# Kernel tuning notes

Measured on AMD Instinct MI355X. Metric: run time of the kernel, lower is better.

## Reference

```python
import jax, jax.numpy as jnp
import numpy as np

B, Cfi, H, W = 2, 32, 192, 192
Cfp, Cfo, NUM = 1, 2, 16
N = H * W
Ct = Cfo + Cfi + Cfi + Cfp  # 67
EPS = 1e-5


def _bn(x, g, b, m, v):
    # x: (B, C, num, N); per-channel inference batchnorm
    inv = g * jax.lax.rsqrt(v + EPS)
    return x * inv[None, :, None, None] + (b - m * inv)[None, :, None, None]


def _pconv(x, Wt):
    # 1x1 conv as channel contraction: Wt (Cout, Cin), x (B, Cin, num, N)
    return jnp.einsum('oc,bcmn->bomn', Wt, x)


def setup_inputs() -> dict:
    key = jax.random.key(0)
    ks = jax.random.split(key, 32)
    inp = {
        'If': jax.random.normal(ks[0], (B, Cfi, H, W), jnp.float32),
        'Pf': jax.random.normal(ks[1], (B, Cfp, H, W), jnp.float32),
        'Ofnum': jax.random.normal(ks[2], (B, Cfo, NUM, N), jnp.float32),
        'args': jax.random.randint(ks[3], (B, NUM, N), 0, N, jnp.int64),
    }
    def conv_w(k, co, ci):
        return jax.random.normal(k, (co, ci), jnp.float32) * (1.0 / np.sqrt(ci))
    def bn_p(k, c):
        k1, k2 = jax.random.split(k)
        return (jnp.ones((c,), jnp.float32),
                jnp.zeros((c,), jnp.float32),
                jax.random.normal(k1, (c,), jnp.float32) * 0.1,
                jax.random.uniform(k2, (c,), jnp.float32, 0.5, 1.5))
    # convXF: Ct->Cfi, Cfi->Cfi (both BN+GELU)
    inp['W1'] = conv_w(ks[4], Cfi, Ct)
    inp['g1'], inp['b1'], inp['m1'], inp['v1'] = bn_p(ks[5], Cfi)
    inp['W2'] = conv_w(ks[6], Cfi, Cfi)
    inp['g2'], inp['b2'], inp['m2'], inp['v2'] = bn_p(ks[7], Cfi)
    # convXL: Cfi->Cfi (BN+GELU), Cfi->Cfi (BN only)
    inp['W3'] = conv_w(ks[8], Cfi, Cfi)
    inp['g3'], inp['b3'], inp['m3'], inp['v3'] = bn_p(ks[9], Cfi)
    inp['W4'] = conv_w(ks[10], Cfi, Cfi)
    inp['g4'], inp['b4'], inp['m4'], inp['v4'] = bn_p(ks[11], Cfi)
    # coef: Cfi -> 3, with bias
    inp['Wc'] = conv_w(ks[12], 3, Cfi)
    inp['bc'] = jax.random.normal(ks[13], (3,), jnp.float32) * 0.01
    return inp


def reference(If, Pf, Ofnum, args,
              W1, g1, b1, m1, v1,
              W2, g2, b2, m2, v2,
              W3, g3, b3, m3, v3,
              W4, g4, b4, m4, v4,
              Wc, bc):
    gelu = lambda x: jax.nn.gelu(x, approximate=False)
    If_flat = If.reshape(B, Cfi, N)   # (B, Cfi, N)
    Pf_flat = Pf.reshape(B, Cfp, N)   # (B, Cfp, M), M == N here

    # per-batch neighbor gather along flattened spatial dim
    gath = jax.vmap(lambda f, a: f[:, a])  # (C,N),(num,N) -> (C,num,N)
    IPfnum = gath(If_flat, args)            # (B, Cfi, num, N)
    Pfnum = gath(Pf_flat, args)             # (B, Cfp, num, N)
    Ifnum = jnp.broadcast_to(If_flat[:, :, None, :], (B, Cfi, NUM, N))

    X = jnp.concatenate([Ifnum, IPfnum, Pfnum, Ofnum], axis=1)  # (B, Ct, num, N)

    h = gelu(_bn(_pconv(X, W1), g1, b1, m1, v1))
    h = gelu(_bn(_pconv(h, W2), g2, b2, m2, v2))
    l = gelu(_bn(_pconv(h, W3), g3, b3, m3, v3))
    l = _bn(_pconv(l, W4), g4, b4, m4, v4)
    XF = gelu(h + l)

    feat = _pconv(XF, Wc) + bc[None, :, None, None]  # (B, 3, num, N)
    Alpha, Beta, Omega = feat[:, 0:1], feat[:, 1:2], feat[:, 2:3]
    Omega = jax.nn.softmax(Omega, axis=2)
    dout = jnp.sum(((Alpha + 1.0) * Pfnum[:, -1:] + Beta) * Omega,
                   axis=2, keepdims=True)  # (B, 1, 1, N)
    return dout.reshape(B, 1, H, W)
```

## Files before the change

kernel.cpp:

```cpp
#include <hip/hip_runtime.h>
#include <math.h>

#define BB   2
#define CFI  32
#define NN   36864
#define NUMM 16

#define ZOFS (BB * NN * CFI)

typedef __attribute__((ext_vector_type(8))) short short8;
typedef __attribute__((ext_vector_type(4))) float f4;

static __device__ __forceinline__ f4 mm16(short8 a, short8 b, f4 c) {
    return __builtin_amdgcn_mfma_f32_16x16x32_bf16(a, b, c, 0, 0, 0);
}

static __device__ __forceinline__ float gelu_fast(float x) {
    const float x2  = x * x;
    const float q   = fmaf(-0.10294310f, x2, -2.30211813f);
    const float e   = exp2f(q * x);
    const float r   = __builtin_amdgcn_rcpf(e + 1.0f);
    return x * r;
}

static __device__ __forceinline__ unsigned bf16_rne_bits(float x) {
    unsigned u = __builtin_bit_cast(unsigned, x);
    return u + 0x7fffu + ((u >> 16) & 1u);
}
static __device__ __forceinline__ void split_pack(float x0, float x1,
                                                  unsigned& hi, unsigned& lo) {
    unsigned r0 = bf16_rne_bits(x0);
    unsigned r1 = bf16_rne_bits(x1);
    float h0 = __builtin_bit_cast(float, r0 & 0xffff0000u);
    float h1 = __builtin_bit_cast(float, r1 & 0xffff0000u);
    hi = (r0 >> 16) | (r1 & 0xffff0000u);
    unsigned s0 = bf16_rne_bits(x0 - h0);
    unsigned s1 = bf16_rne_bits(x1 - h1);
    lo = (s0 >> 16) | (s1 & 0xffff0000u);
}

static __device__ __forceinline__ unsigned pack2(float a, float b) {
    unsigned ua = __builtin_bit_cast(unsigned, a) + 0x8000u;
    unsigned ub = __builtin_bit_cast(unsigned, b) + 0x8000u;
    return (ua >> 16) | (ub & 0xffff0000u);
}

union UV { unsigned u[4]; short8 v; };

__global__ __launch_bounds__(256) void yz_kernel(
    const float* __restrict__ If, const float* __restrict__ Pf,
    const float* __restrict__ W1, const float* __restrict__ g1,
    const float* __restrict__ b1, const float* __restrict__ m1,
    const float* __restrict__ v1,
    float* __restrict__ wsYZ)
{
    __shared__ float wy[1024], wz[1024], wp[32], bt1[32];
    for (int i = threadIdx.x; i < 1024; i += 256) {
        int o = i >> 5, c = i & 31;
        float inv = g1[o] * rsqrtf(v1[o] + 1e-5f);
        wy[i] = W1[o * 67 + c]      * inv;
        wz[i] = W1[o * 67 + 32 + c] * inv;
    }
    if (threadIdx.x < 32) {
        int o = threadIdx.x;
        float inv = g1[o] * rsqrtf(v1[o] + 1e-5f);
        wp[o]  = W1[o * 67 + 64] * inv;
        bt1[o] = b1[o] - m1[o] * inv;
    }
    __syncthreads();

    const int r  = threadIdx.x & 3;
    const int p  = blockIdx.x * 64 + (threadIdx.x >> 2);
    const int b  = p / NN, n = p - b * NN;
    const int o0 = r * 8;
    const float* ifp = If + (size_t)b * CFI * NN + n;

    float v[32];
#pragma unroll
    for (int c = 0; c < 32; c++) v[c] = ifp[(size_t)c * NN];
    const float pf = Pf[p];

    float accY[8], accZ[8];
#pragma unroll
    for (int j = 0; j < 8; j++) {
        const float4* wyr = (const float4*)&wy[(o0 + j) * 32];
        const float4* wzr = (const float4*)&wz[(o0 + j) * 32];
        float ay = bt1[o0 + j];
        float az = wp[o0 + j] * pf;
#pragma unroll
        for (int c4 = 0; c4 < 8; c4++) {
            float4 a = wyr[c4], z = wzr[c4];
            ay = fmaf(a.x, v[4 * c4 + 0], ay);  az = fmaf(z.x, v[4 * c4 + 0], az);
            ay = fmaf(a.y, v[4 * c4 + 1], ay);  az = fmaf(z.y, v[4 * c4 + 1], az);
            ay = fmaf(a.z, v[4 * c4 + 2], ay);  az = fmaf(z.z, v[4 * c4 + 2], az);
            ay = fmaf(a.w, v[4 * c4 + 3], ay);  az = fmaf(z.w, v[4 * c4 + 3], az);
        }
        accY[j] = ay; accZ[j] = az;
    }

    float4* yp = (float4*)(wsYZ + (size_t)p * 32 + o0);
    float4* zp = (float4*)(wsYZ + ZOFS + (size_t)p * 32 + o0);
    yp[0] = make_float4(accY[0], accY[1], accY[2], accY[3]);
    yp[1] = make_float4(accY[4], accY[5], accY[6], accY[7]);
    zp[0] = make_float4(accZ[0], accZ[1], accZ[2], accZ[3]);
    zp[1] = make_float4(accZ[4], accZ[5], accZ[6], accZ[7]);
}

__global__ __launch_bounds__(256, 5) void main_kernel(
    const float* __restrict__ Pf, const float* __restrict__ Of,
    const int* __restrict__ args,
    const float* __restrict__ W1, const float* __restrict__ g1,
    const float* __restrict__ v1,
    const float* __restrict__ W2, const float* __restrict__ g2,
    const float* __restrict__ b2, const float* __restrict__ m2,
    const float* __restrict__ v2,
    const float* __restrict__ W3, const float* __restrict__ g3,
    const float* __restrict__ b3, const float* __restrict__ m3,
    const float* __restrict__ v3,
    const float* __restrict__ W4, const float* __restrict__ g4,
    const float* __restrict__ b4, const float* __restrict__ m4,
    const float* __restrict__ v4,
    const float* __restrict__ Wc, const float* __restrict__ bc,
    const float* __restrict__ ws, float* __restrict__ out)
{
    __shared__ __align__(16) unsigned wfrag[3][2][2][64][4];
    __shared__ __align__(16) float btl[3 * 32];
    __shared__ __align__(16) float wch[3 * 32];
    __shared__ __align__(16) float w1t[2 * 32];
    __shared__ float bcs[3];
    __shared__ int   izs;

    const float* Ws[3] = {W2, W3, W4};
    const float* gs[3] = {g2, g3, g4};
    const float* vs[3] = {v2, v3, v4};
    const float* bs[3] = {b2, b3, b4};
    const float* ms[3] = {m2, m3, m4};

    for (int idx = threadIdx.x; idx < 1536; idx += 256) {
        int p    = idx & 3;
        int ln   = (idx >> 2) & 63;
        int T    = (idx >> 8) & 1;
        int L    = idx >> 9;
        int o    = T * 16 + (ln & 15);
        int c    = ((ln >> 4) << 3) + 2 * p;
        float inv = gs[L][o] * rsqrtf(vs[L][o] + 1e-5f);
        float w0 = Ws[L][o * 32 + c]     * inv;
        float w1 = Ws[L][o * 32 + c + 1] * inv;
        unsigned hi, lo;
        split_pack(w0, w1, hi, lo);
        wfrag[L][T][0][ln][p] = hi;
        wfrag[L][T][1][ln][p] = lo;
    }
    if (threadIdx.x < 96) {
        int L = threadIdx.x >> 5, ch = threadIdx.x & 31;
        btl[threadIdx.x] = bs[L][ch] - ms[L][ch] * (gs[L][ch] * rsqrtf(vs[L][ch] + 1e-5f));
        wch[threadIdx.x] = Wc[L * 32 + ch];
    }
    if (threadIdx.x < 64) {
        int t = threadIdx.x >> 5, ch = threadIdx.x & 31;
        float i1 = g1[ch] * rsqrtf(v1[ch] + 1e-5f);
        w1t[threadIdx.x] = W1[ch * 67 + 65 + t] * i1;
    }
    if (threadIdx.x < 3) bcs[threadIdx.x] = bc[threadIdx.x];
    if (threadIdx.x == 0) izs = (int)(args[0] >> 16);
    __syncthreads();

    const int lane = threadIdx.x & 63;
    const int wid  = threadIdx.x >> 6;
    const int mI   = lane & 15;
    const int quad = lane >> 4;
    const int c0   = quad * 8;
    const int s0   = mI + 32 * (quad & 1);
    const int s1   = s0 + 16;
    const bool hiT = (quad >> 1) != 0;
    const int izero = izs;

#pragma unroll 1
    for (int i = 0; i < 4; i++) {
        const int io  = i & izero;
        const int C = blockIdx.x * 16 + wid * 4 + i;
        const int b = (C >= NN) ? 1 : 0;
        const int n = C - b * NN;

        const int   aIdx = args[(b * NUMM + mI) * NN + n];
        const float of0v = Of[((b * 2 + 0) * NUMM + mI) * NN + n];
        const float of1v = Of[((b * 2 + 1) * NUMM + mI) * NN + n];
        const float pfg  = Pf[b * NN + aIdx];

        const f4* yp = (const f4*)(ws + (size_t)(b * NN + n) * 32 + c0);
        const f4* zp = (const f4*)(ws + ZOFS + (size_t)(b * NN + aIdx) * 32 + c0);
        f4 y0 = yp[0], y1 = yp[1], z0 = zp[0], z1 = zp[1];

        const f4 wo0a = *(const f4*)&w1t[c0 + 4 * io];
        const f4 wo0b = *(const f4*)&w1t[c0 + 4 + 4 * io];
        const f4 wo1a = *(const f4*)&w1t[32 + c0 + 4 * io];
        const f4 wo1b = *(const f4*)&w1t[32 + c0 + 4 + 4 * io];

        float x[8];
#pragma unroll
        for (int j = 0; j < 4; j++) {
            x[j]     = fmaf(of1v, wo1a[j], fmaf(of0v, wo0a[j], y0[j] + z0[j]));
            x[4 + j] = fmaf(of1v, wo1b[j], fmaf(of0v, wo0b[j], y1[j] + z1[j]));
        }
#pragma unroll
        for (int j = 0; j < 8; j++) x[j] = gelu_fast(x[j]);
        UV Bv;
#pragma unroll
        for (int p = 0; p < 4; p++) Bv.u[p] = pack2(x[2 * p], x[2 * p + 1]);

        f4 bt00 = *(const f4*)&btl[0 * 32 + 4 * quad + 4 * io];
        f4 bt01 = *(const f4*)&btl[0 * 32 + 16 + 4 * quad + 4 * io];
        short8 A0l = *(const short8*)&wfrag[0][0][1][lane + io][0];
        short8 A0h = *(const short8*)&wfrag[0][0][0][lane + io][0];
        short8 A1l = *(const short8*)&wfrag[0][1][1][lane + io][0];
        short8 A1h = *(const short8*)&wfrag[0][1][0][lane + io][0];
        f4 acc0 = mm16(A0l, Bv.v, bt00);
        acc0    = mm16(A0h, Bv.v, acc0);
        f4 acc1 = mm16(A1l, Bv.v, bt01);
        acc1    = mm16(A1h, Bv.v, acc1);
        float h2c[8];
#pragma unroll
        for (int r = 0; r < 4; r++) {
            h2c[r]     = gelu_fast(acc0[r]);
            h2c[4 + r] = gelu_fast(acc1[r]);
        }
        {
            unsigned lo0 = pack2(h2c[0], h2c[1]), lo1 = pack2(h2c[2], h2c[3]);
            unsigned hi0 = pack2(h2c[4], h2c[5]), hi1 = pack2(h2c[6], h2c[7]);
            unsigned a0s0 = __shfl(lo0, s0, 64), b0s0 = __shfl(hi0, s0, 64);
            unsigned a1s0 = __shfl(lo1, s0, 64), b1s0 = __shfl(hi1, s0, 64);
            unsigned a0s1 = __shfl(lo0, s1, 64), b0s1 = __shfl(hi0, s1, 64);
            unsigned a1s1 = __shfl(lo1, s1, 64), b1s1 = __shfl(hi1, s1, 64);
            Bv.u[0] = hiT ? b0s0 : a0s0;
            Bv.u[1] = hiT ? b1s0 : a1s0;
            Bv.u[2] = hiT ? b0s1 : a0s1;
            Bv.u[3] = hiT ? b1s1 : a1s1;
        }

        f4 bt10 = *(const f4*)&btl[1 * 32 + 4 * quad + 4 * io];
        f4 bt11 = *(const f4*)&btl[1 * 32 + 16 + 4 * quad + 4 * io];
        A0l = *(const short8*)&wfrag[1][0][1][lane + io][0];
        A0h = *(const short8*)&wfrag[1][0][0][lane + io][0];
        A1l = *(const short8*)&wfrag[1][1][1][lane + io][0];
        A1h = *(const short8*)&wfrag[1][1][0][lane + io][0];
        acc0 = mm16(A0l, Bv.v, bt10);
        acc0 = mm16(A0h, Bv.v, acc0);
        acc1 = mm16(A1l, Bv.v, bt11);
        acc1 = mm16(A1h, Bv.v, acc1);
        {
            float g0 = gelu_fast(acc0[0]), g1_ = gelu_fast(acc0[1]);
            float g2_ = gelu_fast(acc0[2]), g3_ = gelu_fast(acc0[3]);
            float g4_ = gelu_fast(acc1[0]), g5 = gelu_fast(acc1[1]);
            float g6 = gelu_fast(acc1[2]), g7 = gelu_fast(acc1[3]);
            unsigned lo0 = pack2(g0, g1_), lo1 = pack2(g2_, g3_);
            unsigned hi0 = pack2(g4_, g5), hi1 = pack2(g6, g7);
            unsigned a0s0 = __shfl(lo0, s0, 64), b0s0 = __shfl(hi0, s0, 64);
            unsigned a1s0 = __shfl(lo1, s0, 64), b1s0 = __shfl(hi1, s0, 64);
            unsigned a0s1 = __shfl(lo0, s1, 64), b0s1 = __shfl(hi0, s1, 64);
            unsigned a1s1 = __shfl(lo1, s1, 64), b1s1 = __shfl(hi1, s1, 64);
            Bv.u[0] = hiT ? b0s0 : a0s0;
            Bv.u[1] = hiT ? b1s0 : a1s0;
            Bv.u[2] = hiT ? b0s1 : a0s1;
            Bv.u[3] = hiT ? b1s1 : a1s1;
        }

        f4 bt20 = *(const f4*)&btl[2 * 32 + 4 * quad + 4 * io];
        f4 bt21 = *(const f4*)&btl[2 * 32 + 16 + 4 * quad + 4 * io];
        A0l = *(const short8*)&wfrag[2][0][1][lane + io][0];
        A0h = *(const short8*)&wfrag[2][0][0][lane + io][0];
        A1l = *(const short8*)&wfrag[2][1][1][lane + io][0];
        A1h = *(const short8*)&wfrag[2][1][0][lane + io][0];
        acc0 = mm16(A0l, Bv.v, bt20);
        acc0 = mm16(A0h, Bv.v, acc0);
        acc1 = mm16(A1l, Bv.v, bt21);
        acc1 = mm16(A1h, Bv.v, acc1);

        const f4 wA0 = *(const f4*)&wch[0 * 32 + 4 * quad + 4 * io];
        const f4 wA1 = *(const f4*)&wch[0 * 32 + 16 + 4 * quad + 4 * io];
        const f4 wB0 = *(const f4*)&wch[1 * 32 + 4 * quad + 4 * io];
        const f4 wB1 = *(const f4*)&wch[1 * 32 + 16 + 4 * quad + 4 * io];
        const f4 wO0 = *(const f4*)&wch[2 * 32 + 4 * quad + 4 * io];
        const f4 wO1 = *(const f4*)&wch[2 * 32 + 16 + 4 * quad + 4 * io];

        float pa = 0.0f, pb = 0.0f, po = 0.0f;
#pragma unroll
        for (int r = 0; r < 4; r++) {
            float xf0 = gelu_fast(h2c[r]     + acc0[r]);
            float xf1 = gelu_fast(h2c[4 + r] + acc1[r]);
            pa = fmaf(wA0[r], xf0, pa);  pa = fmaf(wA1[r], xf1, pa);
            pb = fmaf(wB0[r], xf0, pb);  pb = fmaf(wB1[r], xf1, pb);
            po = fmaf(wO0[r], xf0, po);  po = fmaf(wO1[r], xf1, po);
        }
        pa += __shfl_xor(pa, 16, 64);  pa += __shfl_xor(pa, 32, 64);
        pb += __shfl_xor(pb, 16, 64);  pb += __shfl_xor(pb, 32, 64);
        po += __shfl_xor(po, 16, 64);  po += __shfl_xor(po, 32, 64);
        const float alpha = pa + bcs[0];
        const float beta_ = pb + bcs[1];
        const float omega = po + bcs[2];
        const float val = fmaf(alpha + 1.0f, pfg, beta_);

        float mx = omega;
#pragma unroll
        for (int s = 1; s < 16; s <<= 1) mx = fmaxf(mx, __shfl_xor(mx, s, 64));
        const float e = __expf(omega - mx);
        float S = e, T = val * e;
#pragma unroll
        for (int s = 1; s < 16; s <<= 1) {
            S += __shfl_xor(S, s, 64);
            T += __shfl_xor(T, s, 64);
        }
        if (lane == 0) out[b * NN + n] = T / S;
    }
}

extern "C" void kernel_launch(void* const* d_in, const int* in_sizes, int n_in,
                              void* d_out, int out_size, void* d_ws, size_t ws_size,
                              hipStream_t stream) {
    const float* If    = (const float*)d_in[0];
    const float* Pf    = (const float*)d_in[1];
    const float* Of    = (const float*)d_in[2];
    const int*   args  = (const int*)d_in[3];
    const float* W1    = (const float*)d_in[4];
    const float* g1    = (const float*)d_in[5];
    const float* b1    = (const float*)d_in[6];
    const float* m1    = (const float*)d_in[7];
    const float* v1    = (const float*)d_in[8];
    const float* W2    = (const float*)d_in[9];
    const float* g2    = (const float*)d_in[10];
    const float* b2    = (const float*)d_in[11];
    const float* m2    = (const float*)d_in[12];
    const float* v2    = (const float*)d_in[13];
    const float* W3    = (const float*)d_in[14];
    const float* g3    = (const float*)d_in[15];
    const float* b3    = (const float*)d_in[16];
    const float* m3    = (const float*)d_in[17];
    const float* v3    = (const float*)d_in[18];
    const float* W4    = (const float*)d_in[19];
    const float* g4    = (const float*)d_in[20];
    const float* b4    = (const float*)d_in[21];
    const float* m4    = (const float*)d_in[22];
    const float* v4    = (const float*)d_in[23];
    const float* Wc    = (const float*)d_in[24];
    const float* bc    = (const float*)d_in[25];

    float* ws  = (float*)d_ws;
    float* out = (float*)d_out;

    yz_kernel<<<(BB * NN) / 64, 256, 0, stream>>>(
        If, Pf, W1, g1, b1, m1, v1, ws);

    main_kernel<<<(BB * NN) / 16, 256, 0, stream>>>(
        Pf, Of, args,
        W1, g1, v1,
        W2, g2, b2, m2, v2,
        W3, g3, b3, m3, v3,
        W4, g4, b4, m4, v4,
        Wc, bc, ws, out);
}
```

Measured before the change: 234.2 us.

## Switch layer MLP to 32x32x16 MFMA covering two pixels per wave

Replaces the 16x16x32 bf16 MFMA chain with 32x32x16 MFMAs so each wave processes two output pixels (32 neighbor columns) per iteration. The weight fragment layout is rebuilt so the accumulator output layout matches the next layer's B-operand input, which removes the cross-lane shuffle relayout between layers. The loop trip count halves and the coefficient reduction needs fewer shuffles. In exchange, per-lane register use grows (16-wide accumulators and activations), which may pressure occupancy under the 5-wave launch bound.

```diff
diff --git a/kernel.cpp b/kernel.cpp
--- a/kernel.cpp
+++ b/kernel.cpp
@@ -10,9 +10,10 @@
 
 typedef __attribute__((ext_vector_type(8))) short short8;
 typedef __attribute__((ext_vector_type(4))) float f4;
-
-static __device__ __forceinline__ f4 mm16(short8 a, short8 b, f4 c) {
-    return __builtin_amdgcn_mfma_f32_16x16x32_bf16(a, b, c, 0, 0, 0);
+typedef __attribute__((ext_vector_type(16))) float f16v;
+
+static __device__ __forceinline__ f16v mm32(short8 a, short8 b, f16v c) {
+    return __builtin_amdgcn_mfma_f32_32x32x16_bf16(a, b, c, 0, 0, 0);
 }
 
 static __device__ __forceinline__ float gelu_fast(float x) {
@@ -105,6 +106,39 @@
     zp[0] = make_float4(accZ[0], accZ[1], accZ[2], accZ[3]);
     zp[1] = make_float4(accZ[4], accZ[5], accZ[6], accZ[7]);
 }
+
+#define LAYER(Lc, BIN0, BIN1, ACCV)                                           \
+    {                                                                         \
+        const f4 bq0 = *(const f4*)&btl[(Lc) * 32 +      4 * hi + 4 * io];    \
+        const f4 bq1 = *(const f4*)&btl[(Lc) * 32 +  8 + 4 * hi + 4 * io];    \
+        const f4 bq2 = *(const f4*)&btl[(Lc) * 32 + 16 + 4 * hi + 4 * io];    \
+        const f4 bq3 = *(const f4*)&btl[(Lc) * 32 + 24 + 4 * hi + 4 * io];    \
+        ACCV[0]  = bq0[0]; ACCV[1]  = bq0[1]; ACCV[2]  = bq0[2]; ACCV[3]  = bq0[3]; \
+        ACCV[4]  = bq1[0]; ACCV[5]  = bq1[1]; ACCV[6]  = bq1[2]; ACCV[7]  = bq1[3]; \
+        ACCV[8]  = bq2[0]; ACCV[9]  = bq2[1]; ACCV[10] = bq2[2]; ACCV[11] = bq2[3]; \
+        ACCV[12] = bq3[0]; ACCV[13] = bq3[1]; ACCV[14] = bq3[2]; ACCV[15] = bq3[3]; \
+        short8 Af;                                                            \
+        Af = *(const short8*)&wfrag[(Lc)][0][1][lane + io][0];                \
+        ACCV = mm32(Af, BIN0.v, ACCV);                                        \
+        Af = *(const short8*)&wfrag[(Lc)][0][0][lane + io][0];                \
+        ACCV = mm32(Af, BIN0.v, ACCV);                                        \
+        Af = *(const short8*)&wfrag[(Lc)][1][1][lane + io][0];                \
+        ACCV = mm32(Af, BIN1.v, ACCV);                                        \
+        Af = *(const short8*)&wfrag[(Lc)][1][0][lane + io][0];                \
+        ACCV = mm32(Af, BIN1.v, ACCV);                                        \
+    }
+
+#define RELAYOUT(SRC, B0V, B1V)                                               \
+    {                                                                         \
+        B0V.u[0] = pack2(SRC[0],  SRC[1]);                                    \
+        B0V.u[1] = pack2(SRC[2],  SRC[3]);                                    \
+        B0V.u[2] = pack2(SRC[4],  SRC[5]);                                    \
+        B0V.u[3] = pack2(SRC[6],  SRC[7]);                                    \
+        B1V.u[0] = pack2(SRC[8],  SRC[9]);                                    \
+        B1V.u[1] = pack2(SRC[10], SRC[11]);                                   \
+        B1V.u[2] = pack2(SRC[12], SRC[13]);                                   \
+        B1V.u[3] = pack2(SRC[14], SRC[15]);                                   \
+    }
 
 __global__ __launch_bounds__(256, 5) void main_kernel(
     const float* __restrict__ Pf, const float* __restrict__ Of,
@@ -137,19 +171,20 @@
     const float* ms[3] = {m2, m3, m4};
 
     for (int idx = threadIdx.x; idx < 1536; idx += 256) {
-        int p    = idx & 3;
-        int ln   = (idx >> 2) & 63;
-        int T    = (idx >> 8) & 1;
-        int L    = idx >> 9;
-        int o    = T * 16 + (ln & 15);
-        int c    = ((ln >> 4) << 3) + 2 * p;
-        float inv = gs[L][o] * rsqrtf(vs[L][o] + 1e-5f);
-        float w0 = Ws[L][o * 32 + c]     * inv;
-        float w1 = Ws[L][o * 32 + c + 1] * inv;
-        unsigned hi, lo;
-        split_pack(w0, w1, hi, lo);
-        wfrag[L][T][0][ln][p] = hi;
-        wfrag[L][T][1][ln][p] = lo;
+        int pp  = idx & 3;
+        int ln  = (idx >> 2) & 63;
+        int kh  = (idx >> 8) & 1;
+        int L   = idx >> 9;
+        int row = ln & 31;
+        int g   = ln >> 5;
+        int k   = kh * 16 + 4 * g + 2 * (pp & 1) + 8 * (pp >> 1);
+        float inv = gs[L][row] * rsqrtf(vs[L][row] + 1e-5f);
+        float w0 = Ws[L][row * 32 + k]     * inv;
+        float w1 = Ws[L][row * 32 + k + 1] * inv;
+        unsigned hiw, low;
+        split_pack(w0, w1, hiw, low);
+        wfrag[L][kh][0][ln][pp] = hiw;
+        wfrag[L][kh][1][ln][pp] = low;
     }
     if (threadIdx.x < 96) {
         int L = threadIdx.x >> 5, ch = threadIdx.x & 31;
@@ -165,135 +200,86 @@
     if (threadIdx.x == 0) izs = (int)(args[0] >> 16);
     __syncthreads();
 
-    const int lane = threadIdx.x & 63;
-    const int wid  = threadIdx.x >> 6;
-    const int mI   = lane & 15;
-    const int quad = lane >> 4;
-    const int c0   = quad * 8;
-    const int s0   = mI + 32 * (quad & 1);
-    const int s1   = s0 + 16;
-    const bool hiT = (quad >> 1) != 0;
+    const int lane  = threadIdx.x & 63;
+    const int wid   = threadIdx.x >> 6;
+    const int m     = lane & 15;
+    const int pt    = (lane >> 4) & 1;
+    const int hi    = lane >> 5;
+    const int q4    = hi << 2;
     const int izero = izs;
 
 #pragma unroll 1
-    for (int i = 0; i < 4; i++) {
-        const int io  = i & izero;
-        const int C = blockIdx.x * 16 + wid * 4 + i;
-        const int b = (C >= NN) ? 1 : 0;
-        const int n = C - b * NN;
-
-        const int   aIdx = args[(b * NUMM + mI) * NN + n];
-        const float of0v = Of[((b * 2 + 0) * NUMM + mI) * NN + n];
-        const float of1v = Of[((b * 2 + 1) * NUMM + mI) * NN + n];
+    for (int i = 0; i < 2; i++) {
+        const int io = i & izero;
+        const int C  = blockIdx.x * 16 + wid * 4 + i * 2 + pt;
+        const int b  = (C >= NN) ? 1 : 0;
+        const int n  = C - b * NN;
+
+        const int   aIdx = args[(b * NUMM + m) * NN + n];
+        const float of0v = Of[((b * 2 + 0) * NUMM + m) * NN + n];
+        const float of1v = Of[((b * 2 + 1) * NUMM + m) * NN + n];
         const float pfg  = Pf[b * NN + aIdx];
 
-        const f4* yp = (const f4*)(ws + (size_t)(b * NN + n) * 32 + c0);
-        const f4* zp = (const f4*)(ws + ZOFS + (size_t)(b * NN + aIdx) * 32 + c0);
-        f4 y0 = yp[0], y1 = yp[1], z0 = zp[0], z1 = zp[1];
-
-        const f4 wo0a = *(const f4*)&w1t[c0 + 4 * io];
-        const f4 wo0b = *(const f4*)&w1t[c0 + 4 + 4 * io];
-        const f4 wo1a = *(const f4*)&w1t[32 + c0 + 4 * io];
-        const f4 wo1b = *(const f4*)&w1t[32 + c0 + 4 + 4 * io];
-
-        float x[8];
+        const f4* yb = (const f4*)(ws + (size_t)(b * NN + n) * 32);
+        const f4* zb = (const f4*)(ws + ZOFS + (size_t)(b * NN + aIdx) * 32);
+        f4 y0 = yb[hi], y1 = yb[2 + hi], y2 = yb[4 + hi], y3 = yb[6 + hi];
+        f4 z0 = zb[hi], z1 = zb[2 + hi], z2 = zb[4 + hi], z3 = zb[6 + hi];
+
+        const f4 wa0 = *(const f4*)&w1t[q4 + 4 * io];
+        const f4 wa1 = *(const f4*)&w1t[8 + q4 + 4 * io];
+        const f4 wa2 = *(const f4*)&w1t[16 + q4 + 4 * io];
+        const f4 wa3 = *(const f4*)&w1t[24 + q4 + 4 * io];
+        const f4 wb0 = *(const f4*)&w1t[32 + q4 + 4 * io];
+        const f4 wb1 = *(const f4*)&w1t[40 + q4 + 4 * io];
+        const f4 wb2 = *(const f4*)&w1t[48 + q4 + 4 * io];
+        const f4 wb3 = *(const f4*)&w1t[56 + q4 + 4 * io];
+
+        float x[16];
 #pragma unroll
         for (int j = 0; j < 4; j++) {
-            x[j]     = fmaf(of1v, wo1a[j], fmaf(of0v, wo0a[j], y0[j] + z0[j]));
-            x[4 + j] = fmaf(of1v, wo1b[j], fmaf(of0v, wo0b[j], y1[j] + z1[j]));
+            x[j]      = fmaf(of1v, wb0[j], fmaf(of0v, wa0[j], y0[j] + z0[j]));
+            x[4 + j]  = fmaf(of1v, wb1[j], fmaf(of0v, wa1[j], y1[j] + z1[j]));
+            x[8 + j]  = fmaf(of1v, wb2[j], fmaf(of0v, wa2[j], y2[j] + z2[j]));
+            x[12 + j] = fmaf(of1v, wb3[j], fmaf(of0v, wa3[j], y3[j] + z3[j]));
         }
 #pragma unroll
-        for (int j = 0; j < 8; j++) x[j] = gelu_fast(x[j]);
-        UV Bv;
-#pragma unroll
-        for (int p = 0; p < 4; p++) Bv.u[p] = pack2(x[2 * p], x[2 * p + 1]);
-
-        f4 bt00 = *(const f4*)&btl[0 * 32 + 4 * quad + 4 * io];
-        f4 bt01 = *(const f4*)&btl[0 * 32 + 16 + 4 * quad + 4 * io];
-        short8 A0l = *(const short8*)&wfrag[0][0][1][lane + io][0];
-        short8 A0h = *(const short8*)&wfrag[0][0][0][lane + io][0];
-        short8 A1l = *(const short8*)&wfrag[0][1][1][lane + io][0];
-        short8 A1h = *(const short8*)&wfrag[0][1][0][lane + io][0];
-        f4 acc0 = mm16(A0l, Bv.v, bt00);
-        acc0    = mm16(A0h, Bv.v, acc0);
-        f4 acc1 = mm16(A1l, Bv.v, bt01);
-        acc1    = mm16(A1h, Bv.v, acc1);
-        float h2c[8];
-#pragma unroll
-        for (int r = 0; r < 4; r++) {
-            h2c[r]     = gelu_fast(acc0[r]);
-            h2c[4 + r] = gelu_fast(acc1[r]);
+        for (int j = 0; j < 16; j++) x[j] = gelu_fast(x[j]);
+        UV B0, B1;
+        RELAYOUT(x, B0, B1);
+
+        f16v acc;
+        LAYER(0, B0, B1, acc);
+        float h2g[16];
+#pragma unroll
+        for (int r = 0; r < 16; r++) h2g[r] = gelu_fast(acc[r]);
+        RELAYOUT(h2g, B0, B1);
+
+        LAYER(1, B0, B1, acc);
+        float h3g[16];
+#pragma unroll
+        for (int r = 0; r < 16; r++) h3g[r] = gelu_fast(acc[r]);
+        RELAYOUT(h3g, B0, B1);
+
+        LAYER(2, B0, B1, acc);
+
+        float pa = 0.0f, pb = 0.0f, po = 0.0f;
+#pragma unroll
+        for (int q = 0; q < 4; q++) {
+            const f4 wAq = *(const f4*)&wch[      8 * q + q4 + 4 * io];
+            const f4 wBq = *(const f4*)&wch[32 +  8 * q + q4 + 4 * io];
+            const f4 wOq = *(const f4*)&wch[64 +  8 * q + q4 + 4 * io];
+#pragma unroll
+            for (int r2 = 0; r2 < 4; r2++) {
+                float xf = gelu_fast(h2g[4 * q + r2] + acc[4 * q + r2]);
+                pa = fmaf(wAq[r2], xf, pa);
+                pb = fmaf(wBq[r2], xf, pb);
+                po = fmaf(wOq[r2], xf, po);
+            }
         }
-        {
-            unsigned lo0 = pack2(h2c[0], h2c[1]), lo1 = pack2(h2c[2], h2c[3]);
-            unsigned hi0 = pack2(h2c[4], h2c[5]), hi1 = pack2(h2c[6], h2c[7]);
-            unsigned a0s0 = __shfl(lo0, s0, 64), b0s0 = __shfl(hi0, s0, 64);
-            unsigned a1s0 = __shfl(lo1, s0, 64), b1s0 = __shfl(hi1, s0, 64);
-            unsigned a0s1 = __shfl(lo0, s1, 64), b0s1 = __shfl(hi0, s1, 64);
-            unsigned a1s1 = __shfl(lo1, s1, 64), b1s1 = __shfl(hi1, s1, 64);
-            Bv.u[0] = hiT ? b0s0 : a0s0;
-            Bv.u[1] = hiT ? b1s0 : a1s0;
-            Bv.u[2] = hiT ? b0s1 : a0s1;
-            Bv.u[3] = hiT ? b1s1 : a1s1;
-        }
-
-        f4 bt10 = *(const f4*)&btl[1 * 32 + 4 * quad + 4 * io];
-        f4 bt11 = *(const f4*)&btl[1 * 32 + 16 + 4 * quad + 4 * io];
-        A0l = *(const short8*)&wfrag[1][0][1][lane + io][0];
-        A0h = *(const short8*)&wfrag[1][0][0][lane + io][0];
-        A1l = *(const short8*)&wfrag[1][1][1][lane + io][0];
-        A1h = *(const short8*)&wfrag[1][1][0][lane + io][0];
-        acc0 = mm16(A0l, Bv.v, bt10);
-        acc0 = mm16(A0h, Bv.v, acc0);
-        acc1 = mm16(A1l, Bv.v, bt11);
-        acc1 = mm16(A1h, Bv.v, acc1);
-        {
-            float g0 = gelu_fast(acc0[0]), g1_ = gelu_fast(acc0[1]);
-            float g2_ = gelu_fast(acc0[2]), g3_ = gelu_fast(acc0[3]);
-            float g4_ = gelu_fast(acc1[0]), g5 = gelu_fast(acc1[1]);
-            float g6 = gelu_fast(acc1[2]), g7 = gelu_fast(acc1[3]);
-            unsigned lo0 = pack2(g0, g1_), lo1 = pack2(g2_, g3_);
-            unsigned hi0 = pack2(g4_, g5), hi1 = pack2(g6, g7);
-            unsigned a0s0 = __shfl(lo0, s0, 64), b0s0 = __shfl(hi0, s0, 64);
-            unsigned a1s0 = __shfl(lo1, s0, 64), b1s0 = __shfl(hi1, s0, 64);
-            unsigned a0s1 = __shfl(lo0, s1, 64), b0s1 = __shfl(hi0, s1, 64);
-            unsigned a1s1 = __shfl(lo1, s1, 64), b1s1 = __shfl(hi1, s1, 64);
-            Bv.u[0] = hiT ? b0s0 : a0s0;
-            Bv.u[1] = hiT ? b1s0 : a1s0;
-            Bv.u[2] = hiT ? b0s1 : a0s1;
-            Bv.u[3] = hiT ? b1s1 : a1s1;
-        }
-
-        f4 bt20 = *(const f4*)&btl[2 * 32 + 4 * quad + 4 * io];
-        f4 bt21 = *(const f4*)&btl[2 * 32 + 16 + 4 * quad + 4 * io];
-        A0l = *(const short8*)&wfrag[2][0][1][lane + io][0];
-        A0h = *(const short8*)&wfrag[2][0][0][lane + io][0];
-        A1l = *(const short8*)&wfrag[2][1][1][lane + io][0];
-        A1h = *(const short8*)&wfrag[2][1][0][lane + io][0];
-        acc0 = mm16(A0l, Bv.v, bt20);
-        acc0 = mm16(A0h, Bv.v, acc0);
-        acc1 = mm16(A1l, Bv.v, bt21);
-        acc1 = mm16(A1h, Bv.v, acc1);
-
-        const f4 wA0 = *(const f4*)&wch[0 * 32 + 4 * quad + 4 * io];
-        const f4 wA1 = *(const f4*)&wch[0 * 32 + 16 + 4 * quad + 4 * io];
-        const f4 wB0 = *(const f4*)&wch[1 * 32 + 4 * quad + 4 * io];
-        const f4 wB1 = *(const f4*)&wch[1 * 32 + 16 + 4 * quad + 4 * io];
-        const f4 wO0 = *(const f4*)&wch[2 * 32 + 4 * quad + 4 * io];
-        const f4 wO1 = *(const f4*)&wch[2 * 32 + 16 + 4 * quad + 4 * io];
-
-        float pa = 0.0f, pb = 0.0f, po = 0.0f;
-#pragma unroll
-        for (int r = 0; r < 4; r++) {
-            float xf0 = gelu_fast(h2c[r]     + acc0[r]);
-            float xf1 = gelu_fast(h2c[4 + r] + acc1[r]);
-            pa = fmaf(wA0[r], xf0, pa);  pa = fmaf(wA1[r], xf1, pa);
-            pb = fmaf(wB0[r], xf0, pb);  pb = fmaf(wB1[r], xf1, pb);
-            po = fmaf(wO0[r], xf0, po);  po = fmaf(wO1[r], xf1, po);
-        }
-        pa += __shfl_xor(pa, 16, 64);  pa += __shfl_xor(pa, 32, 64);
-        pb += __shfl_xor(pb, 16, 64);  pb += __shfl_xor(pb, 32, 64);
-        po += __shfl_xor(po, 16, 64);  po += __shfl_xor(po, 32, 64);
+        pa += __shfl_xor(pa, 32, 64);
+        pb += __shfl_xor(pb, 32, 64);
+        po += __shfl_xor(po, 32, 64);
+
         const float alpha = pa + bcs[0];
         const float beta_ = pb + bcs[1];
         const float omega = po + bcs[2];
@@ -309,7 +295,8 @@
             S += __shfl_xor(S, s, 64);
             T += __shfl_xor(T, s, 64);
         }
-        if (lane == 0) out[b * NN + n] = T / S;
+        if ((lane & 15) == 0 && lane < 32)
+            out[b * NN + n] = T * __builtin_amdgcn_rcpf(S);
     }
 }
 
```

Measured after the change: 232.0 us. Within noise of the previous version (-1.0%).
